# Performance work log

Measured on AMD Instinct MI355X. Metric: run time of the kernel, lower is better.

## Reference

```python
import jax, jax.numpy as jnp
import numpy as np

KS = 3           # kernel size (conv1, conv2, deform conv)
PAD = 1          # k//2 padding for the dense convs and deform zero-padding
DIM = 256
B, H, W = 4, 64, 64
N = KS * KS      # number of sampling points per output pixel


def conv2d(x, w, b=None, pad=PAD, stride=1):
    out = jax.lax.conv_general_dilated(
        x, w, (stride, stride), [(pad, pad), (pad, pad)],
        dimension_numbers=('NCHW', 'OIHW', 'NCHW'))
    if b is not None:
        out = out + b[None, :, None, None]
    return out


def deform_conv(x, p_w, p_b, dw):
    # DeformConv2d (deform-conv-v2 style, modulation=False)
    b, c, h, w = x.shape
    offset = conv2d(x, p_w, p_b, pad=1)                     # (b, 2N, h, w)
    xp = jnp.pad(x, ((0, 0), (0, 0), (PAD, PAD), (PAD, PAD)))
    Hp, Wp = h + 2 * PAD, w + 2 * PAD

    # kernel-relative offsets p_n: rows first, then cols (row-major flatten)
    r = jnp.arange(-(KS - 1) // 2, (KS - 1) // 2 + 1, dtype=x.dtype)
    pnx, pny = jnp.meshgrid(r, r, indexing='ij')
    p_n = jnp.concatenate([pnx.ravel(), pny.ravel()])       # (2N,)

    # base grid p_0 starts at 1 (consistent with zero padding of 1)
    gy, gx = jnp.meshgrid(jnp.arange(1, h + 1, dtype=x.dtype),
                          jnp.arange(1, w + 1, dtype=x.dtype), indexing='ij')
    p0 = jnp.concatenate([jnp.tile(gy[..., None], (1, 1, N)),
                          jnp.tile(gx[..., None], (1, 1, N))], axis=-1)  # (h,w,2N)

    p = jnp.transpose(offset, (0, 2, 3, 1)) + p_n + p0      # (b,h,w,2N)
    px, py = p[..., :N], p[..., N:]
    fx, fy = jnp.floor(px), jnp.floor(py)
    qlx = jnp.clip(fx, 0, Hp - 1)
    qly = jnp.clip(fy, 0, Wp - 1)
    qrx = jnp.clip(fx + 1, 0, Hp - 1)
    qry = jnp.clip(fy + 1, 0, Wp - 1)
    px = jnp.clip(px, 0, Hp - 1)
    py = jnp.clip(py, 0, Wp - 1)

    # bilinear weights
    g_lt = (1 + qlx - px) * (1 + qly - py)
    g_rb = (1 - qrx + px) * (1 - qry + py)
    g_lb = (1 + qlx - px) * (1 - qry + py)
    g_rt = (1 - qrx + px) * (1 + qly - py)

    xf = xp.reshape(b, c, Hp * Wp)

    def gather(qx, qy):
        idx = (qx.astype(jnp.int32) * Wp + qy.astype(jnp.int32)).reshape(b, -1)
        return jax.vmap(lambda xb, ib: xb[:, ib])(xf, idx).reshape(b, c, h, w, N)

    x_off = (g_lt[:, None] * gather(qlx, qly) + g_rb[:, None] * gather(qrx, qry)
           + g_lb[:, None] * gather(qlx, qry) + g_rt[:, None] * gather(qrx, qly))

    # (b,c,h,w,N) -> (b,c,h*ks,w*ks): kernel row expands h, kernel col expands w
    x_off = x_off.reshape(b, c, h, w, KS, KS).transpose(0, 1, 2, 4, 3, 5)
    x_off = x_off.reshape(b, c, h * KS, w * KS)
    return conv2d(x_off, dw, None, pad=0, stride=KS)       # (b, c, h, w)


def setup_inputs() -> dict:
    key = jax.random.key(0)
    ks = jax.random.split(key, 8)
    s = 1.0 / np.sqrt(DIM * KS * KS)
    return {
        'x':   jax.random.normal(ks[0], (B, DIM, H, W), jnp.float32),
        'w1':  jax.random.normal(ks[1], (DIM, DIM, KS, KS), jnp.float32) * s,
        'b1':  jax.random.normal(ks[2], (DIM,), jnp.float32) * 0.01,
        'w2':  jax.random.normal(ks[3], (DIM, DIM, KS, KS), jnp.float32) * s,
        'b2':  jax.random.normal(ks[4], (DIM,), jnp.float32) * 0.01,
        'p_w': jax.random.normal(ks[5], (2 * N, DIM, 3, 3), jnp.float32) * (0.05 * s),
        'p_b': jnp.zeros((2 * N,), jnp.float32),
        'dw':  jax.random.normal(ks[6], (DIM, DIM, KS, KS), jnp.float32) * s,
    }


def reference(x, w1, b1, w2, b2, p_w, p_b, dw):
    res = jax.nn.relu(conv2d(x, w1, b1, pad=PAD))   # conv1 + ReLU
    res = res + x                                   # residual 1
    res = conv2d(res, w2, b2, pad=PAD)              # conv2
    res = deform_conv(res, p_w, p_b, dw)            # deformable conv
    return res + x                                  # residual 2
```

## Files before the change

### kernel.cpp

```cpp
#include <hip/hip_runtime.h>

#define HW 64
#define NB 4
#define CH 256

typedef __attribute__((address_space(1))) const void* gptr_t;
typedef __attribute__((address_space(3))) void* lptr_t;
typedef __attribute__((ext_vector_type(8))) short bf8v;
typedef __attribute__((ext_vector_type(4))) float f32x4;

__device__ __forceinline__ void gll16(const void* g, void* l) {
  __builtin_amdgcn_global_load_lds((gptr_t)g, (lptr_t)l, 16, 0, 0);
}
__device__ __forceinline__ ushort f2b(float f) {
  union { float f; uint u; } v; v.f = f;
  uint r = v.u + 0x7FFF + ((v.u >> 16) & 1);
  return (ushort)(r >> 16);
}
__device__ __forceinline__ float b2f(ushort b) {
  union { uint u; float f; } v; v.u = ((uint)b) << 16;
  return v.f;
}

__global__ __launch_bounds__(256) void zero_borders_k(
    ushort* __restrict__ xpad, ushort* __restrict__ res1, ushort* __restrict__ res2)
{
  const int buf = blockIdx.x >> 2, b = blockIdx.x & 3;
  ushort* base = (buf == 0 ? xpad : buf == 1 ? res1 : res2) + (size_t)b * 4356 * 256;
  uint4 z; z.x = 0; z.y = 0; z.z = 0; z.w = 0;
  for (int u = threadIdx.x; u < 260 * 32; u += 256) {
    const int p = u >> 5, k = u & 31;
    int r, cc;
    if (p < 66)       { r = 0;       cc = p; }
    else if (p < 132) { r = 65;      cc = p - 66; }
    else if (p < 196) { r = p - 131; cc = 0; }
    else              { r = p - 195; cc = 65; }
    *(uint4*)&base[((size_t)r * 66 + cc) * 256 + k * 8] = z;
  }
}

__global__ __launch_bounds__(256) void pack_x_k(
    const float* __restrict__ x, ushort* __restrict__ xpad)
{
  __shared__ float tile[64][261];
  const int t = threadIdx.x, b = blockIdx.x >> 6, i = blockIdx.x & 63;
  const int wave = t >> 6, l = t & 63;
  const float* src = x + (size_t)b * CH * 4096 + (size_t)i * 64;
  for (int cc = 0; cc < 64; ++cc) {
    const int c = cc * 4 + wave;
    tile[l][c] = src[(size_t)c * 4096 + l];
  }
  __syncthreads();
  const int c0 = (t & 31) * 8;
  #pragma unroll
  for (int jj = 0; jj < 8; ++jj) {
    const int j = (t >> 5) + jj * 8;
    const float4 v0 = *(const float4*)&tile[j][c0];
    const float4 v1 = *(const float4*)&tile[j][c0 + 4];
    uint4 o;
    o.x = (uint)f2b(v0.x) | ((uint)f2b(v0.y) << 16);
    o.y = (uint)f2b(v0.z) | ((uint)f2b(v0.w) << 16);
    o.z = (uint)f2b(v1.x) | ((uint)f2b(v1.y) << 16);
    o.w = (uint)f2b(v1.z) | ((uint)f2b(v1.w) << 16);
    *(uint4*)&xpad[((size_t)b * 4356 + (i + 1) * 66 + (j + 1)) * 256 + c0] = o;
  }
}

__global__ __launch_bounds__(256) void pack_w_k(
    const float* __restrict__ w1, const float* __restrict__ w2,
    const float* __restrict__ dw, const float* __restrict__ pw,
    const float* __restrict__ pb,
    ushort* __restrict__ wpk1, ushort* __restrict__ wpk2,
    ushort* __restrict__ dwpk, ushort* __restrict__ wpkO, float* __restrict__ pbias)
{
  const int id = blockIdx.x * 256 + threadIdx.x;
  if (id < 3 * 73728) {
    const int tsel = id / 73728, r = id % 73728;
    const int kc = r & 3, o = (r >> 2) & 255, ct = r >> 10;
    const int cb = ct / 9, tap = ct % 9;
    const float* w = (tsel == 0) ? w1 : (tsel == 1) ? w2 : dw;
    const float* s = w + ((size_t)o * CH + cb * 32 + kc * 8) * 9 + tap;
    ushort* d = ((tsel == 0) ? wpk1 : (tsel == 1) ? wpk2 : dwpk) + (size_t)r * 8;
    #pragma unroll
    for (int j = 0; j < 8; ++j) d[j] = f2b(s[j * 9]);
  } else if (id < 3 * 73728 + 9216) {
    const int r = id - 3 * 73728;
    const int kc = r & 3, o = (r >> 2) & 31, ct = r >> 7;
    const int cb = ct / 9, tap = ct % 9;
    ushort* d = wpkO + (size_t)r * 8;
    if (o < 18) {
      const float* s = pw + ((size_t)o * CH + cb * 32 + kc * 8) * 9 + tap;
      #pragma unroll
      for (int j = 0; j < 8; ++j) d[j] = f2b(s[j * 9]);
    } else {
      #pragma unroll
      for (int j = 0; j < 8; ++j) d[j] = 0;
    }
  }
  if (id < 32) pbias[id] = (id < 18) ? pb[id] : 0.f;
}

template<int OTOT, int OUTMODE>
__global__ __launch_bounds__(256, 4) void conv_mfma(
    const ushort* __restrict__ apad, const ushort* __restrict__ wpk,
    const float* __restrict__ bias, const float* __restrict__ xres,
    void* __restrict__ outp)
{
  __shared__ __align__(16) ushort patch[2][6336];
  const int t = threadIdx.x, wave = t >> 6, l = t & 63;
  const int ot  = (OTOT == 256) ? (blockIdx.x >> 8) : 0;
  const int rem = blockIdx.x & 255;
  const int b = rem >> 6, i = rem & 63;
  const int ln = l & 15, kc8 = (l >> 4) * 8;

  constexpr int FO = (OTOT == 256) ? 1 : 2;
  constexpr int FP = (OTOT == 256) ? 4 : 1;
  const int oS  = (OTOT == 256) ? (ot * 64 + wave * 16) : 0;
  const int pxB = (OTOT == 256) ? 0 : (wave * 16);

  const ushort* rowbase = apad + ((size_t)(b * 66 + i) * 66) * 256;

  f32x4 acc[FO][FP];
  #pragma unroll
  for (int a = 0; a < FO; ++a)
    #pragma unroll
    for (int d = 0; d < FP; ++d) acc[a][d] = (f32x4){0.f, 0.f, 0.f, 0.f};

  #define STAGE(buf, cb)                                                        \
    _Pragma("unroll")                                                           \
    for (int it = 0; it < 4; ++it) {                                            \
      const int e = t + it * 256;                                               \
      if (it < 3 || t < 24) {                                                   \
        const int r = e / 264, u = e - r * 264;                                 \
        const ushort* s = rowbase + ((size_t)(r * 66) + (u >> 2)) * 256         \
                          + (cb) * 32 + (u & 3) * 8;                            \
        gll16(s, (ushort*)&patch[buf][0] + (size_t)e * 8);                      \
      }                                                                         \
    }

  STAGE(0, 0)
  for (int cb = 0; cb < 8; ++cb) {
    __syncthreads();
    bf8v wfr[9][FO];
    #pragma unroll
    for (int tap = 0; tap < 9; ++tap)
      #pragma unroll
      for (int fo = 0; fo < FO; ++fo)
        wfr[tap][fo] = *(const bf8v*)&wpk[((size_t)((cb * 9 + tap) * OTOT) + oS + fo * 16 + ln) * 32 + kc8];
    if (cb < 7) { STAGE((cb + 1) & 1, cb + 1) }
    const ushort* pbuf = &patch[cb & 1][0];
    __builtin_amdgcn_s_setprio(1);
    #pragma unroll
    for (int tap = 0; tap < 9; ++tap) {
      const int ky = tap / 3, kx = tap % 3;
      bf8v pf[FP];
      #pragma unroll
      for (int fp = 0; fp < FP; ++fp) {
        const int px = pxB + fp * 16 + ln;
        pf[fp] = *(const bf8v*)&pbuf[ky * 2112 + (px + kx) * 32 + kc8];
      }
      #pragma unroll
      for (int fo = 0; fo < FO; ++fo)
        #pragma unroll
        for (int fp = 0; fp < FP; ++fp)
          acc[fo][fp] = __builtin_amdgcn_mfma_f32_16x16x32_bf16(wfr[tap][fo], pf[fp], acc[fo][fp], 0, 0, 0);
    }
    __builtin_amdgcn_s_setprio(0);
  }
  #undef STAGE

  #pragma unroll
  for (int fo = 0; fo < FO; ++fo) {
    #pragma unroll
    for (int fp = 0; fp < FP; ++fp) {
      const f32x4 a = acc[fo][fp];
      const int o = oS + fo * 16 + (l >> 4) * 4;
      const int j = pxB + fp * 16 + ln;
      const float4 bv = *(const float4*)&bias[o];
      float v0 = a[0] + bv.x, v1 = a[1] + bv.y, v2 = a[2] + bv.z, v3 = a[3] + bv.w;
      if (OUTMODE == 0) {
        const size_t xb = (((size_t)b * CH + o) * HW + i) * HW + j;
        v0 = fmaxf(v0, 0.f) + xres[xb];
        v1 = fmaxf(v1, 0.f) + xres[xb + 4096];
        v2 = fmaxf(v2, 0.f) + xres[xb + 8192];
        v3 = fmaxf(v3, 0.f) + xres[xb + 12288];
      }
      if (OUTMODE == 2) {
        float* op = (float*)outp + ((size_t)b * 4096 + i * 64 + j) * 32 + o;
        float4 r; r.x = v0; r.y = v1; r.z = v2; r.w = v3;
        *(float4*)op = r;
      } else {
        ushort* op = (ushort*)outp + ((size_t)b * 4356 + (i + 1) * 66 + (j + 1)) * 256 + o;
        ushort4 s; s.x = f2b(v0); s.y = f2b(v1); s.z = f2b(v2); s.w = f2b(v3);
        *(ushort4*)op = s;
      }
    }
  }
}

__global__ __launch_bounds__(1024, 4) void deform_mfma(
    const ushort* __restrict__ res2pad, const float* __restrict__ offs,
    const ushort* __restrict__ dwpk, const float* __restrict__ x,
    float* __restrict__ out)
{
  __shared__ __align__(16) ushort samp[2][18432];
  __shared__ __align__(16) int    tbl_i[576 * 4];
  __shared__ __align__(16) float  tbl_w[576 * 4];

  const int t = threadIdx.x, wave = t >> 6, l = t & 63;
  const int b = blockIdx.x >> 6, i = blockIdx.x & 63;
  const int ln = l & 15, kc8 = (l >> 4) * 8;
  const int oS = wave * 16;

  if (t < 576) {
    const int n = t >> 6, j = t & 63;
    const int ki = n / 3, kj = n % 3;
    const float offr = offs[((size_t)b * 4096 + i * 64 + j) * 32 + n];
    const float offc = offs[((size_t)b * 4096 + i * 64 + j) * 32 + 9 + n];
    const float prow = offr + (float)(ki - 1) + (float)(i + 1);
    const float pcol = offc + (float)(kj - 1) + (float)(j + 1);
    const float fx = floorf(prow), fy = floorf(pcol);
    const float qlx = fminf(fmaxf(fx, 0.f), 65.f);
    const float qly = fminf(fmaxf(fy, 0.f), 65.f);
    const float qrx = fminf(fmaxf(fx + 1.f, 0.f), 65.f);
    const float qry = fminf(fmaxf(fy + 1.f, 0.f), 65.f);
    const float pr  = fminf(fmaxf(prow, 0.f), 65.f);
    const float pc  = fminf(fmaxf(pcol, 0.f), 65.f);
    tbl_i[t * 4 + 0] = (int)qlx * 66 + (int)qly;
    tbl_i[t * 4 + 1] = (int)qrx * 66 + (int)qry;
    tbl_i[t * 4 + 2] = (int)qlx * 66 + (int)qry;
    tbl_i[t * 4 + 3] = (int)qrx * 66 + (int)qly;
    tbl_w[t * 4 + 0] = (1.f + qlx - pr) * (1.f + qly - pc);
    tbl_w[t * 4 + 1] = (1.f - qrx + pr) * (1.f - qry + pc);
    tbl_w[t * 4 + 2] = (1.f + qlx - pr) * (1.f - qry + pc);
    tbl_w[t * 4 + 3] = (1.f - qrx + pr) * (1.f + qly - pc);
  }

  f32x4 acc[4];
  #pragma unroll
  for (int a = 0; a < 4; ++a) acc[a] = (f32x4){0.f, 0.f, 0.f, 0.f};

  const ushort* res2b = res2pad + (size_t)b * 4356 * 256;
  __syncthreads();

  #define SAMPLE_DIRECT(u_, cb_, buf_) {                                        \
    const int e = (u_) >> 2, i16 = (u_) & 3;                                    \
    const int4 iv = *(const int4*)&tbl_i[e * 4];                                \
    const ushort* base = res2b + (cb_) * 32 + i16 * 8;                          \
    const bf8v c0 = *(const bf8v*)(base + (size_t)iv.x * 256);                  \
    const bf8v c1 = *(const bf8v*)(base + (size_t)iv.y * 256);                  \
    const bf8v c2 = *(const bf8v*)(base + (size_t)iv.z * 256);                  \
    const bf8v c3 = *(const bf8v*)(base + (size_t)iv.w * 256);                  \
    const float4 gv = *(const float4*)&tbl_w[e * 4];                            \
    bf8v ob;                                                                    \
    _Pragma("unroll")                                                           \
    for (int jj = 0; jj < 8; ++jj) {                                            \
      const float s = gv.x * b2f((ushort)c0[jj]) + gv.y * b2f((ushort)c1[jj])   \
                    + gv.z * b2f((ushort)c2[jj]) + gv.w * b2f((ushort)c3[jj]);  \
      ob[jj] = (short)f2b(s);                                                   \
    }                                                                           \
    *(bf8v*)&samp[buf_][(size_t)(u_) * 8] = ob;                                 \
  }

  #pragma unroll
  for (int k = 0; k < 3; ++k) {
    if (k < 2 || t < 256) {
      const int u = t + k * 1024;
      SAMPLE_DIRECT(u, 0, 0)
    }
  }
  __syncthreads();

  bf8v cr[2][4];
  for (int cb = 0; cb < 8; ++cb) {
    bf8v bfr[9];
    #pragma unroll
    for (int tap = 0; tap < 9; ++tap)
      bfr[tap] = *(const bf8v*)&dwpk[((size_t)(cb * 9 + tap) * 256 + oS + ln) * 32 + kc8];

    if (cb < 7) {
      #pragma unroll
      for (int k = 0; k < 2; ++k) {
        const int u = t + k * 1024;
        const int e = u >> 2, i16 = u & 3;
        const int4 iv = *(const int4*)&tbl_i[e * 4];
        const ushort* base = res2b + (cb + 1) * 32 + i16 * 8;
        cr[k][0] = *(const bf8v*)(base + (size_t)iv.x * 256);
        cr[k][1] = *(const bf8v*)(base + (size_t)iv.y * 256);
        cr[k][2] = *(const bf8v*)(base + (size_t)iv.z * 256);
        cr[k][3] = *(const bf8v*)(base + (size_t)iv.w * 256);
      }
    }

    const ushort* sb = &samp[cb & 1][0];
    __builtin_amdgcn_s_setprio(1);
    #pragma unroll
    for (int tap = 0; tap < 9; ++tap) {
      #pragma unroll
      for (int fp = 0; fp < 4; ++fp) {
        const bf8v af = *(const bf8v*)&sb[(tap * 64 + fp * 16 + ln) * 32 + kc8];
        acc[fp] = __builtin_amdgcn_mfma_f32_16x16x32_bf16(af, bfr[tap], acc[fp], 0, 0, 0);
      }
    }
    __builtin_amdgcn_s_setprio(0);

    if (cb < 7) {
      const int buf = (cb + 1) & 1;
      #pragma unroll
      for (int k = 0; k < 2; ++k) {
        const int u = t + k * 1024;
        const int e = u >> 2;
        const float4 gv = *(const float4*)&tbl_w[e * 4];
        bf8v ob;
        #pragma unroll
        for (int jj = 0; jj < 8; ++jj) {
          const float s = gv.x * b2f((ushort)cr[k][0][jj]) + gv.y * b2f((ushort)cr[k][1][jj])
                        + gv.z * b2f((ushort)cr[k][2][jj]) + gv.w * b2f((ushort)cr[k][3][jj]);
          ob[jj] = (short)f2b(s);
        }
        *(bf8v*)&samp[buf][(size_t)u * 8] = ob;
      }
      if (t < 256) {
        const int u = 2048 + t;
        SAMPLE_DIRECT(u, cb + 1, buf)
      }
    }
    __syncthreads();
  }
  #undef SAMPLE_DIRECT

  #pragma unroll
  for (int fp = 0; fp < 4; ++fp) {
    const f32x4 a = acc[fp];
    const int o = oS + ln;
    const int j0 = fp * 16 + (l >> 4) * 4;
    const size_t base = (((size_t)b * CH + o) * HW + i) * HW + j0;
    const float4 xv = *(const float4*)&x[base];
    float4 r; r.x = a[0] + xv.x; r.y = a[1] + xv.y; r.z = a[2] + xv.z; r.w = a[3] + xv.w;
    *(float4*)&out[base] = r;
  }
}

extern "C" void kernel_launch(void* const* d_in, const int* in_sizes, int n_in,
                              void* d_out, int out_size, void* d_ws, size_t ws_size,
                              hipStream_t stream) {
  (void)in_sizes; (void)n_in; (void)out_size; (void)ws_size;
  const float* x  = (const float*)d_in[0];
  const float* w1 = (const float*)d_in[1];
  const float* b1 = (const float*)d_in[2];
  const float* w2 = (const float*)d_in[3];
  const float* b2 = (const float*)d_in[4];
  const float* pw = (const float*)d_in[5];
  const float* pb = (const float*)d_in[6];
  const float* dw = (const float*)d_in[7];
  float* out = (float*)d_out;

  char* w = (char*)d_ws;
  size_t off = 0;
  auto carve = [&](size_t bytes) { char* p = w + off; off += (bytes + 255) & ~(size_t)255; return p; };
  ushort* xpad  = (ushort*)carve(8929280);
  ushort* res1  = (ushort*)carve(8929280);
  ushort* res2  = (ushort*)carve(8929280);
  ushort* wpk1  = (ushort*)carve(1179648);
  ushort* wpk2  = (ushort*)carve(1179648);
  ushort* wpkO  = (ushort*)carve(147456);
  ushort* dwpk  = (ushort*)carve(1179648);
  float*  pbias = (float*) carve(256);
  float*  offs  = (float*) carve(2097152);

  zero_borders_k<<<12, 256, 0, stream>>>(xpad, res1, res2);
  pack_w_k<<<900, 256, 0, stream>>>(w1, w2, dw, pw, pb, wpk1, wpk2, dwpk, wpkO, pbias);
  pack_x_k<<<256, 256, 0, stream>>>(x, xpad);
  conv_mfma<256, 0><<<1024, 256, 0, stream>>>(xpad, wpk1, b1, x, res1);
  conv_mfma<256, 1><<<1024, 256, 0, stream>>>(res1, wpk2, b2, nullptr, res2);
  conv_mfma<32, 2><<<256, 256, 0, stream>>>(res2, wpkO, pbias, nullptr, offs);
  deform_mfma<<<NB * HW, 1024, 0, stream>>>(res2, offs, dwpk, x, out);
}
```

Measured before the change: 140.4 us.

## Keep deform sampling indices and weights in registers and use packed bf16 convert

Each thread now computes its own bilinear indices and weights straight from the offsets and keeps them in registers, replacing the shared-memory lookup tables and the barrier that followed them. Indices are pre-scaled to byte offsets, and the bf16-to-float unpack plus float-to-bf16 pack use shift/mask and the hardware v_cvt_pk_bf16_f32 instruction instead of scalar rounding code. The intent is to cut shared-memory traffic and ALU work in the sampling step. It costs more registers per thread and some repeated index math, and the rounding may differ slightly from the software round-to-nearest-even.

```diff
diff --git a/kernel.cpp b/kernel.cpp
--- a/kernel.cpp
+++ b/kernel.cpp
@@ -17,9 +17,32 @@
   uint r = v.u + 0x7FFF + ((v.u >> 16) & 1);
   return (ushort)(r >> 16);
 }
-__device__ __forceinline__ float b2f(ushort b) {
-  union { uint u; float f; } v; v.u = ((uint)b) << 16;
-  return v.f;
+__device__ __forceinline__ uint cvt_pk_bf16(float lo, float hi) {
+  uint r;
+  asm("v_cvt_pk_bf16_f32 %0, %1, %2" : "=v"(r) : "v"(lo), "v"(hi));
+  return r;
+}
+__device__ __forceinline__ float asf(uint u) {
+  union { uint u; float f; } v; v.u = u; return v.f;
+}
+
+__device__ __forceinline__ void combine_store(
+    const uint4& c0, const uint4& c1, const uint4& c2, const uint4& c3,
+    const float4& gw, ushort* dst)
+{
+  uint o[4];
+  const uint* p0 = (const uint*)&c0; const uint* p1 = (const uint*)&c1;
+  const uint* p2 = (const uint*)&c2; const uint* p3 = (const uint*)&c3;
+  #pragma unroll
+  for (int w = 0; w < 4; ++w) {
+    const float lo = gw.x * asf(p0[w] << 16) + gw.y * asf(p1[w] << 16)
+                   + gw.z * asf(p2[w] << 16) + gw.w * asf(p3[w] << 16);
+    const float hi = gw.x * asf(p0[w] & 0xffff0000u) + gw.y * asf(p1[w] & 0xffff0000u)
+                   + gw.z * asf(p2[w] & 0xffff0000u) + gw.w * asf(p3[w] & 0xffff0000u);
+    o[w] = cvt_pk_bf16(lo, hi);
+  }
+  uint4 r; r.x = o[0]; r.y = o[1]; r.z = o[2]; r.w = o[3];
+  *(uint4*)dst = r;
 }
 
 __global__ __launch_bounds__(256) void zero_borders_k(
@@ -58,10 +81,10 @@
     const float4 v0 = *(const float4*)&tile[j][c0];
     const float4 v1 = *(const float4*)&tile[j][c0 + 4];
     uint4 o;
-    o.x = (uint)f2b(v0.x) | ((uint)f2b(v0.y) << 16);
-    o.y = (uint)f2b(v0.z) | ((uint)f2b(v0.w) << 16);
-    o.z = (uint)f2b(v1.x) | ((uint)f2b(v1.y) << 16);
-    o.w = (uint)f2b(v1.z) | ((uint)f2b(v1.w) << 16);
+    o.x = cvt_pk_bf16(v0.x, v0.y);
+    o.y = cvt_pk_bf16(v0.z, v0.w);
+    o.z = cvt_pk_bf16(v1.x, v1.y);
+    o.w = cvt_pk_bf16(v1.z, v1.w);
     *(uint4*)&xpad[((size_t)b * 4356 + (i + 1) * 66 + (j + 1)) * 256 + c0] = o;
   }
 }
@@ -204,91 +227,78 @@
     float* __restrict__ out)
 {
   __shared__ __align__(16) ushort samp[2][18432];
-  __shared__ __align__(16) int    tbl_i[576 * 4];
-  __shared__ __align__(16) float  tbl_w[576 * 4];
 
   const int t = threadIdx.x, wave = t >> 6, l = t & 63;
   const int b = blockIdx.x >> 6, i = blockIdx.x & 63;
   const int ln = l & 15, kc8 = (l >> 4) * 8;
   const int oS = wave * 16;
 
-  if (t < 576) {
-    const int n = t >> 6, j = t & 63;
-    const int ki = n / 3, kj = n % 3;
-    const float offr = offs[((size_t)b * 4096 + i * 64 + j) * 32 + n];
-    const float offc = offs[((size_t)b * 4096 + i * 64 + j) * 32 + 9 + n];
-    const float prow = offr + (float)(ki - 1) + (float)(i + 1);
-    const float pcol = offc + (float)(kj - 1) + (float)(j + 1);
-    const float fx = floorf(prow), fy = floorf(pcol);
-    const float qlx = fminf(fmaxf(fx, 0.f), 65.f);
-    const float qly = fminf(fmaxf(fy, 0.f), 65.f);
-    const float qrx = fminf(fmaxf(fx + 1.f, 0.f), 65.f);
-    const float qry = fminf(fmaxf(fy + 1.f, 0.f), 65.f);
-    const float pr  = fminf(fmaxf(prow, 0.f), 65.f);
-    const float pc  = fminf(fmaxf(pcol, 0.f), 65.f);
-    tbl_i[t * 4 + 0] = (int)qlx * 66 + (int)qly;
-    tbl_i[t * 4 + 1] = (int)qrx * 66 + (int)qry;
-    tbl_i[t * 4 + 2] = (int)qlx * 66 + (int)qry;
-    tbl_i[t * 4 + 3] = (int)qrx * 66 + (int)qly;
-    tbl_w[t * 4 + 0] = (1.f + qlx - pr) * (1.f + qly - pc);
-    tbl_w[t * 4 + 1] = (1.f - qrx + pr) * (1.f - qry + pc);
-    tbl_w[t * 4 + 2] = (1.f + qlx - pr) * (1.f - qry + pc);
-    tbl_w[t * 4 + 3] = (1.f - qrx + pr) * (1.f + qly - pc);
-  }
-
-  f32x4 acc[4];
-  #pragma unroll
-  for (int a = 0; a < 4; ++a) acc[a] = (f32x4){0.f, 0.f, 0.f, 0.f};
-
-  const ushort* res2b = res2pad + (size_t)b * 4356 * 256;
-  __syncthreads();
-
-  #define SAMPLE_DIRECT(u_, cb_, buf_) {                                        \
-    const int e = (u_) >> 2, i16 = (u_) & 3;                                    \
-    const int4 iv = *(const int4*)&tbl_i[e * 4];                                \
-    const ushort* base = res2b + (cb_) * 32 + i16 * 8;                          \
-    const bf8v c0 = *(const bf8v*)(base + (size_t)iv.x * 256);                  \
-    const bf8v c1 = *(const bf8v*)(base + (size_t)iv.y * 256);                  \
-    const bf8v c2 = *(const bf8v*)(base + (size_t)iv.z * 256);                  \
-    const bf8v c3 = *(const bf8v*)(base + (size_t)iv.w * 256);                  \
-    const float4 gv = *(const float4*)&tbl_w[e * 4];                            \
-    bf8v ob;                                                                    \
-    _Pragma("unroll")                                                           \
-    for (int jj = 0; jj < 8; ++jj) {                                            \
-      const float s = gv.x * b2f((ushort)c0[jj]) + gv.y * b2f((ushort)c1[jj])   \
-                    + gv.z * b2f((ushort)c2[jj]) + gv.w * b2f((ushort)c3[jj]);  \
-      ob[jj] = (short)f2b(s);                                                   \
-    }                                                                           \
-    *(bf8v*)&samp[buf_][(size_t)(u_) * 8] = ob;                                 \
-  }
-
+  int4   ivr[3];
+  float4 gwr[3];
   #pragma unroll
   for (int k = 0; k < 3; ++k) {
     if (k < 2 || t < 256) {
-      const int u = t + k * 1024;
-      SAMPLE_DIRECT(u, 0, 0)
+      const int u = (k < 2) ? (t + k * 1024) : (2048 + t);
+      const int e = u >> 2, tap = e >> 6, j = e & 63;
+      const int ki = tap / 3, kj = tap % 3;
+      const float offr = offs[((size_t)(b * 64 + i) * 64 + j) * 32 + tap];
+      const float offc = offs[((size_t)(b * 64 + i) * 64 + j) * 32 + 9 + tap];
+      const float prow = offr + (float)(ki - 1) + (float)(i + 1);
+      const float pcol = offc + (float)(kj - 1) + (float)(j + 1);
+      const float fx = floorf(prow), fy = floorf(pcol);
+      const float qlx = fminf(fmaxf(fx, 0.f), 65.f);
+      const float qly = fminf(fmaxf(fy, 0.f), 65.f);
+      const float qrx = fminf(fmaxf(fx + 1.f, 0.f), 65.f);
+      const float qry = fminf(fmaxf(fy + 1.f, 0.f), 65.f);
+      const float pr  = fminf(fmaxf(prow, 0.f), 65.f);
+      const float pc  = fminf(fmaxf(pcol, 0.f), 65.f);
+      ivr[k].x = ((int)qlx * 66 + (int)qly) * 512;
+      ivr[k].y = ((int)qrx * 66 + (int)qry) * 512;
+      ivr[k].z = ((int)qlx * 66 + (int)qry) * 512;
+      ivr[k].w = ((int)qrx * 66 + (int)qly) * 512;
+      gwr[k].x = (1.f + qlx - pr) * (1.f + qly - pc);
+      gwr[k].y = (1.f - qrx + pr) * (1.f - qry + pc);
+      gwr[k].z = (1.f + qlx - pr) * (1.f - qry + pc);
+      gwr[k].w = (1.f + qlx - pr) * 0.f + (1.f - qrx + pr) * (1.f + qly - pc);
+    }
+  }
+
+  f32x4 acc[4];
+  #pragma unroll
+  for (int a = 0; a < 4; ++a) acc[a] = (f32x4){0.f, 0.f, 0.f, 0.f};
+
+  const char* res2b = (const char*)(res2pad + (size_t)b * 4356 * 256);
+  const int laneoff = (t & 3) * 16;
+
+  #pragma unroll
+  for (int k = 0; k < 3; ++k) {
+    if (k < 2 || t < 256) {
+      const int u = (k < 2) ? (t + k * 1024) : (2048 + t);
+      const char* gb = res2b + laneoff;
+      const uint4 c0 = *(const uint4*)(gb + ivr[k].x);
+      const uint4 c1 = *(const uint4*)(gb + ivr[k].y);
+      const uint4 c2 = *(const uint4*)(gb + ivr[k].z);
+      const uint4 c3 = *(const uint4*)(gb + ivr[k].w);
+      combine_store(c0, c1, c2, c3, gwr[k], &samp[0][(size_t)u * 8]);
     }
   }
   __syncthreads();
 
-  bf8v cr[2][4];
   for (int cb = 0; cb < 8; ++cb) {
     bf8v bfr[9];
     #pragma unroll
     for (int tap = 0; tap < 9; ++tap)
       bfr[tap] = *(const bf8v*)&dwpk[((size_t)(cb * 9 + tap) * 256 + oS + ln) * 32 + kc8];
 
+    uint4 cr[2][4];
+    const char* gb = res2b + (cb + 1) * 64 + laneoff;
     if (cb < 7) {
       #pragma unroll
       for (int k = 0; k < 2; ++k) {
-        const int u = t + k * 1024;
-        const int e = u >> 2, i16 = u & 3;
-        const int4 iv = *(const int4*)&tbl_i[e * 4];
-        const ushort* base = res2b + (cb + 1) * 32 + i16 * 8;
-        cr[k][0] = *(const bf8v*)(base + (size_t)iv.x * 256);
-        cr[k][1] = *(const bf8v*)(base + (size_t)iv.y * 256);
-        cr[k][2] = *(const bf8v*)(base + (size_t)iv.z * 256);
-        cr[k][3] = *(const bf8v*)(base + (size_t)iv.w * 256);
+        cr[k][0] = *(const uint4*)(gb + ivr[k].x);
+        cr[k][1] = *(const uint4*)(gb + ivr[k].y);
+        cr[k][2] = *(const uint4*)(gb + ivr[k].z);
+        cr[k][3] = *(const uint4*)(gb + ivr[k].w);
       }
     }
 
@@ -306,28 +316,20 @@
 
     if (cb < 7) {
       const int buf = (cb + 1) & 1;
-      #pragma unroll
-      for (int k = 0; k < 2; ++k) {
-        const int u = t + k * 1024;
-        const int e = u >> 2;
-        const float4 gv = *(const float4*)&tbl_w[e * 4];
-        bf8v ob;
-        #pragma unroll
-        for (int jj = 0; jj < 8; ++jj) {
-          const float s = gv.x * b2f((ushort)cr[k][0][jj]) + gv.y * b2f((ushort)cr[k][1][jj])
-                        + gv.z * b2f((ushort)cr[k][2][jj]) + gv.w * b2f((ushort)cr[k][3][jj]);
-          ob[jj] = (short)f2b(s);
-        }
-        *(bf8v*)&samp[buf][(size_t)u * 8] = ob;
-      }
+      uint4 d0, d1, d2, d3;
       if (t < 256) {
-        const int u = 2048 + t;
-        SAMPLE_DIRECT(u, cb + 1, buf)
-      }
+        d0 = *(const uint4*)(gb + ivr[2].x);
+        d1 = *(const uint4*)(gb + ivr[2].y);
+        d2 = *(const uint4*)(gb + ivr[2].z);
+        d3 = *(const uint4*)(gb + ivr[2].w);
+      }
+      combine_store(cr[0][0], cr[0][1], cr[0][2], cr[0][3], gwr[0], &samp[buf][(size_t)t * 8]);
+      combine_store(cr[1][0], cr[1][1], cr[1][2], cr[1][3], gwr[1], &samp[buf][(size_t)(t + 1024) * 8]);
+      if (t < 256)
+        combine_store(d0, d1, d2, d3, gwr[2], &samp[buf][(size_t)(2048 + t) * 8]);
     }
     __syncthreads();
   }
-  #undef SAMPLE_DIRECT
 
   #pragma unroll
   for (int fp = 0; fp < 4; ++fp) {
```

Result: slower. 174.2 us (+24.0%).
